# Performance work log

Hardware: AMD Instinct MI355X
Metric: run time of the kernel (lower is better)

Reference implementation:

```python
import jax, jax.numpy as jnp
import numpy as np

ATOMF_LEN = 82
EDGE_DIM = 6
HIDDEN = 10
GNN_DEPTH = 2
N_NODES = 200000
N_EDGES = 6400000


def _lrelu(x):
    return jax.nn.leaky_relu(x, negative_slope=0.1)


def setup_inputs() -> dict:
    key = jax.random.key(0)
    ks = jax.random.split(key, 7)
    vertex = jax.random.normal(ks[0], (N_NODES, ATOMF_LEN), dtype=jnp.float32)
    edge_feat = jax.random.normal(ks[1], (N_EDGES, EDGE_DIM), dtype=jnp.float32)
    src = jax.random.randint(ks[2], (N_EDGES,), 0, N_NODES, dtype=jnp.int32)
    dst = jax.random.randint(ks[3], (N_EDGES,), 0, N_NODES, dtype=jnp.int32)
    # kaiming-uniform-ish init scale (fan_in based)
    weight_init = jax.random.uniform(ks[4], (ATOMF_LEN, HIDDEN), dtype=jnp.float32,
                                     minval=-1.0, maxval=1.0) * (np.sqrt(6.0 / ATOMF_LEN))
    gather_weight = jax.random.uniform(ks[5], (HIDDEN + EDGE_DIM, HIDDEN), dtype=jnp.float32,
                                       minval=-1.0, maxval=1.0) * (np.sqrt(6.0 / (HIDDEN + EDGE_DIM)))
    update_weight = jax.random.uniform(ks[6], (2 * HIDDEN, HIDDEN), dtype=jnp.float32,
                                       minval=-1.0, maxval=1.0) * (np.sqrt(6.0 / (2 * HIDDEN)))
    return {"vertex": vertex, "edge_feat": edge_feat, "src": src, "dst": dst,
            "weight_init": weight_init, "gather_weight": gather_weight,
            "update_weight": update_weight}


def reference(vertex, edge_feat, src, dst, weight_init, gather_weight, update_weight):
    # embedding_: leaky_relu(mm(x, W), 0.1)
    h = _lrelu(vertex @ weight_init)  # [N, HIDDEN]
    n_nodes = vertex.shape[0]
    for _ in range(GNN_DEPTH):
        # gather: per-edge message from source node hidden + edge features
        msg = _lrelu(jnp.concatenate([h[src], edge_feat], axis=1) @ gather_weight)  # [E, HIDDEN]
        # scatter-sum aggregation onto destination nodes
        agg = jax.ops.segment_sum(msg, dst, num_segments=n_nodes)  # [N, HIDDEN]
        # update: combine current hidden with aggregated messages
        h = _lrelu(jnp.concatenate([h, agg], axis=1) @ update_weight)  # [N, HIDDEN]
    return h
```

## Files before the change

kernel.cpp:

```cpp
#include <hip/hip_runtime.h>

#define ATOMF 82
#define EDGE_DIM 6
#define HIDDEN 10
#define ZPAD 16

#define BSHIFT 8
#define BUCKN (1 << BSHIFT)
#define MAXBUCK 1024
#define NB2 256
#define MAXE3 16384

__device__ __forceinline__ float lrelu(float x) { return x > 0.f ? x : 0.1f * x; }

__device__ __forceinline__ unsigned int f2bf(float f) {
    unsigned int u = __float_as_uint(f);
    return (u + 0x7fffu + ((u >> 16) & 1u)) >> 16;
}
__device__ __forceinline__ float bf2f(unsigned int b) {
    return __uint_as_float(b << 16);
}

__global__ void embed_kernel(const float* __restrict__ vertex,
                             const float* __restrict__ W,
                             const float* __restrict__ GW,
                             float* __restrict__ h, unsigned short* __restrict__ z,
                             int n_nodes) {
    __shared__ float w[ATOMF * HIDDEN];
    __shared__ float gwh[HIDDEN * HIDDEN];
    for (int i = threadIdx.x; i < ATOMF * HIDDEN; i += blockDim.x) w[i] = W[i];
    for (int i = threadIdx.x; i < HIDDEN * HIDDEN; i += blockDim.x) gwh[i] = GW[i];
    __syncthreads();
    int node = blockIdx.x * blockDim.x + threadIdx.x;
    if (node >= n_nodes) return;
    const float2* v = (const float2*)(vertex + (long)node * ATOMF);
    float acc[HIDDEN];
#pragma unroll
    for (int j = 0; j < HIDDEN; j++) acc[j] = 0.f;
#pragma unroll 2
    for (int k2 = 0; k2 < ATOMF / 2; k2++) {
        float2 t = v[k2];
#pragma unroll
        for (int j = 0; j < HIDDEN; j++) acc[j] += t.x * w[(2 * k2) * HIDDEN + j];
#pragma unroll
        for (int j = 0; j < HIDDEN; j++) acc[j] += t.y * w[(2 * k2 + 1) * HIDDEN + j];
    }
    float ho[HIDDEN];
    float* out = h + (long)node * HIDDEN;
#pragma unroll
    for (int j = 0; j < HIDDEN; j++) { ho[j] = lrelu(acc[j]); out[j] = ho[j]; }
    float zv[HIDDEN];
#pragma unroll
    for (int j = 0; j < HIDDEN; j++) zv[j] = 0.f;
#pragma unroll
    for (int k = 0; k < HIDDEN; k++) {
        float x = ho[k];
#pragma unroll
        for (int j = 0; j < HIDDEN; j++) zv[j] += x * gwh[k * HIDDEN + j];
    }
    unsigned int* zq = (unsigned int*)(z + (size_t)node * ZPAD);
    int4 pk;
    pk.x = (int)(f2bf(zv[0]) | (f2bf(zv[1]) << 16));
    pk.y = (int)(f2bf(zv[2]) | (f2bf(zv[3]) << 16));
    pk.z = (int)(f2bf(zv[4]) | (f2bf(zv[5]) << 16));
    pk.w = (int)(f2bf(zv[6]) | (f2bf(zv[7]) << 16));
    *(int4*)zq = pk;
    zq[4] = f2bf(zv[8]) | (f2bf(zv[9]) << 16);
}

__global__ __launch_bounds__(512) void hist_kernel(const int* __restrict__ dst,
                                                   int* __restrict__ hist,
                                                   long n_edges, int nbuck) {
    __shared__ int hl[MAXBUCK];
    for (int t = threadIdx.x; t < nbuck; t += 512) hl[t] = 0;
    __syncthreads();
    long per = (n_edges + gridDim.x - 1) / gridDim.x;
    long s = (long)blockIdx.x * per;
    long e = s + per; if (e > n_edges) e = n_edges;
    for (long i = s + threadIdx.x; i < e; i += 512)
        atomicAdd(&hl[dst[i] >> BSHIFT], 1);
    __syncthreads();
    for (int t = threadIdx.x; t < nbuck; t += 512)
        hist[(size_t)t * gridDim.x + blockIdx.x] = hl[t];
}

__global__ __launch_bounds__(1024) void scan_block_sums(const int* __restrict__ in,
                                                        int* __restrict__ partials, int n) {
    __shared__ int ws[16];
    int i = blockIdx.x * 1024 + threadIdx.x;
    int v = (i < n) ? in[i] : 0;
    int lane = threadIdx.x & 63, wid = threadIdx.x >> 6;
    int s = v;
#pragma unroll
    for (int off = 32; off > 0; off >>= 1) s += __shfl_down(s, off, 64);
    if (lane == 0) ws[wid] = s;
    __syncthreads();
    if (threadIdx.x == 0) {
        int t = 0;
#pragma unroll
        for (int k = 0; k < 16; k++) t += ws[k];
        partials[blockIdx.x] = t;
    }
}
__global__ __launch_bounds__(1024) void scan_partials(int* __restrict__ partials, int nb) {
    __shared__ int wsum[16];
    int lane = threadIdx.x & 63, wid = threadIdx.x >> 6;
    int v = (threadIdx.x < nb) ? partials[threadIdx.x] : 0;
    int incl = v;
#pragma unroll
    for (int off = 1; off < 64; off <<= 1) {
        int t = __shfl_up(incl, off, 64);
        if (lane >= off) incl += t;
    }
    if (lane == 63) wsum[wid] = incl;
    __syncthreads();
    if (wid == 0 && lane < 16) {
        int wv = wsum[lane];
        int wincl = wv;
#pragma unroll
        for (int off = 1; off < 16; off <<= 1) {
            int t = __shfl_up(wincl, off, 64);
            if (lane >= off) wincl += t;
        }
        wsum[lane] = wincl - wv;
    }
    __syncthreads();
    if (threadIdx.x < nb) partials[threadIdx.x] = wsum[wid] + (incl - v);
}
__global__ __launch_bounds__(1024) void scan_final(const int* __restrict__ in,
                                                   const int* __restrict__ partials,
                                                   int* __restrict__ out, int n) {
    __shared__ int wsum[16];
    int i = blockIdx.x * 1024 + threadIdx.x;
    int v = (i < n) ? in[i] : 0;
    int lane = threadIdx.x & 63, wid = threadIdx.x >> 6;
    int incl = v;
#pragma unroll
    for (int off = 1; off < 64; off <<= 1) {
        int t = __shfl_up(incl, off, 64);
        if (lane >= off) incl += t;
    }
    if (lane == 63) wsum[wid] = incl;
    __syncthreads();
    if (wid == 0 && lane < 16) {
        int wv = wsum[lane];
        int wincl = wv;
#pragma unroll
        for (int off = 1; off < 16; off <<= 1) {
            int t = __shfl_up(wincl, off, 64);
            if (lane >= off) wincl += t;
        }
        wsum[lane] = wincl - wv;
    }
    __syncthreads();
    if (i <= n) out[i] = partials[blockIdx.x] + wsum[wid] + (incl - v);
}

__global__ __launch_bounds__(512) void part_scatter_kernel(
    const int* __restrict__ src, const int* __restrict__ dst,
    const float* __restrict__ ef, const int* __restrict__ base,
    int4* __restrict__ rec, long n_edges, int nbuck) {
    __shared__ int cur[MAXBUCK];
    for (int t = threadIdx.x; t < nbuck; t += 512)
        cur[t] = base[(size_t)t * gridDim.x + blockIdx.x];
    __syncthreads();
    long per = (n_edges + gridDim.x - 1) / gridDim.x;
    long s = (long)blockIdx.x * per;
    long e = s + per; if (e > n_edges) e = n_edges;
    for (long i = s + threadIdx.x; i < e; i += 512) {
        int d = dst[i];
        int slot = atomicAdd(&cur[d >> BSHIFT], 1);
        const float2* er = (const float2*)(ef + i * (long)EDGE_DIM);
        float2 fa = er[0], fb = er[1], fc = er[2];
        int4 r;
        r.x = src[i] | ((d & (BUCKN - 1)) << 24);
        r.y = (int)(f2bf(fa.x) | (f2bf(fa.y) << 16));
        r.z = (int)(f2bf(fb.x) | (f2bf(fb.y) << 16));
        r.w = (int)(f2bf(fc.x) | (f2bf(fc.y) << 16));
        rec[slot] = r;
    }
}

__global__ __launch_bounds__(256) void bucket_csr_kernel(
    const int* __restrict__ base, const int4* __restrict__ rec_a, int4* __restrict__ rec_b,
    int* __restrict__ offsets, int n_nodes) {
    __shared__ unsigned char lid[MAXE3];
    __shared__ int cnt[BUCKN];
    __shared__ int excl_s[BUCKN];
    __shared__ int cursor[BUCKN];
    int b = blockIdx.x;
    int S = base[(size_t)b * NB2];
    int E = base[(size_t)(b + 1) * NB2];
    int node0 = b << BSHIFT;
    int nn = n_nodes - node0; if (nn > BUCKN) nn = BUCKN;
    cnt[threadIdx.x] = 0;
    __syncthreads();
    int ne = E - S;
    bool fit = (ne <= MAXE3);
    for (int i = threadIdx.x; i < ne; i += 256) {
        int l = (int)((unsigned int)rec_a[S + i].x >> 24);
        if (fit) lid[i] = (unsigned char)l;
        atomicAdd(&cnt[l], 1);
    }
    __syncthreads();
    if (threadIdx.x == 0) {
        int run = 0;
#pragma unroll 4
        for (int l = 0; l < BUCKN; l++) { excl_s[l] = run; run += cnt[l]; }
    }
    __syncthreads();
    if ((int)threadIdx.x < nn) offsets[node0 + threadIdx.x] = S + excl_s[threadIdx.x];
    cursor[threadIdx.x] = excl_s[threadIdx.x];
    if (b == (int)gridDim.x - 1 && threadIdx.x == 0) offsets[n_nodes] = E;
    __syncthreads();
    for (int i = threadIdx.x; i < ne; i += 256) {
        int4 r = rec_a[S + i];
        int l = fit ? (int)lid[i] : (int)((unsigned int)r.x >> 24);
        int q = atomicAdd(&cursor[l], 1);
        rec_b[S + q] = r;
    }
}

__global__ void count_pos_kernel(const int* __restrict__ dst, int* __restrict__ counts,
                                 unsigned short* __restrict__ pos, long n_edges) {
    long e0 = ((long)blockIdx.x * blockDim.x + threadIdx.x) * 4;
    if (e0 + 3 < n_edges) {
        int4 d = *(const int4*)(dst + e0);
        ushort4 p;
        p.x = (unsigned short)atomicAdd(&counts[d.x], 1);
        p.y = (unsigned short)atomicAdd(&counts[d.y], 1);
        p.z = (unsigned short)atomicAdd(&counts[d.z], 1);
        p.w = (unsigned short)atomicAdd(&counts[d.w], 1);
        *(ushort4*)(pos + e0) = p;
    } else {
        for (long e = e0; e < n_edges; e++)
            pos[e] = (unsigned short)atomicAdd(&counts[dst[e]], 1);
    }
}
__global__ void scatter_rec_kernel(const int* __restrict__ src, const int* __restrict__ dst,
                                   const float* __restrict__ ef,
                                   const unsigned short* __restrict__ pos,
                                   const int* __restrict__ offsets,
                                   int4* __restrict__ rec, long n_edges) {
    long e = (long)blockIdx.x * blockDim.x + threadIdx.x;
    if (e >= n_edges) return;
    int d = dst[e];
    int q = offsets[d] + (int)pos[e];
    const float2* er = (const float2*)(ef + e * (long)EDGE_DIM);
    float2 fa = er[0], fb = er[1], fc = er[2];
    int4 r;
    r.x = src[e];
    r.y = (int)(f2bf(fa.x) | (f2bf(fa.y) << 16));
    r.z = (int)(f2bf(fb.x) | (f2bf(fb.y) << 16));
    r.w = (int)(f2bf(fc.x) | (f2bf(fc.y) << 16));
    rec[q] = r;
}

__global__ __launch_bounds__(256) void gather_update_kernel(
    const float* __restrict__ h_in, const unsigned short* __restrict__ z_in,
    const int4* __restrict__ rec, const int* __restrict__ offsets,
    const float* __restrict__ GW, const float* __restrict__ UW,
    float* __restrict__ h_out, unsigned short* __restrict__ z_out,
    int n_nodes, int write_z, unsigned int src_mask) {
    __shared__ float gwh[HIDDEN * HIDDEN];
    __shared__ float gwe[EDGE_DIM * HIDDEN];
    __shared__ float uw[2 * HIDDEN * HIDDEN];
    for (int i = threadIdx.x; i < HIDDEN * HIDDEN; i += 256) gwh[i] = GW[i];
    for (int i = threadIdx.x; i < EDGE_DIM * HIDDEN; i += 256) gwe[i] = GW[HIDDEN * HIDDEN + i];
    for (int i = threadIdx.x; i < 2 * HIDDEN * HIDDEN; i += 256) uw[i] = UW[i];
    __syncthreads();
    int group = threadIdx.x >> 4;
    int sub = threadIdx.x & 15;
    int node = blockIdx.x * 16 + group;
    if (node >= n_nodes) return;
    int off0 = offsets[node], off1 = offsets[node + 1];
    float acc[HIDDEN];
#pragma unroll
    for (int j = 0; j < HIDDEN; j++) acc[j] = 0.f;
    int p = off0 + sub;
    int4 r;
    if (p < off1) r = rec[p];
    while (p < off1) {
        int pn = p + 16;
        int4 rn = r;
        if (pn < off1) rn = rec[pn];
        int sn = (int)((unsigned int)r.x & src_mask);
        const int* zq = (const int*)(z_in + (size_t)sn * ZPAD);
        int4 za = *(const int4*)zq;
        int zb = zq[4];
        float ef[EDGE_DIM];
        unsigned int u0 = (unsigned int)r.y, u1 = (unsigned int)r.z, u2 = (unsigned int)r.w;
        ef[0] = bf2f(u0 & 0xffffu); ef[1] = bf2f(u0 >> 16);
        ef[2] = bf2f(u1 & 0xffffu); ef[3] = bf2f(u1 >> 16);
        ef[4] = bf2f(u2 & 0xffffu); ef[5] = bf2f(u2 >> 16);
        float m[HIDDEN];
#pragma unroll
        for (int j = 0; j < HIDDEN; j++) m[j] = 0.f;
#pragma unroll
        for (int k = 0; k < EDGE_DIM; k++) {
            float x = ef[k];
#pragma unroll
            for (int j = 0; j < HIDDEN; j++) m[j] += x * gwe[k * HIDDEN + j];
        }
        unsigned int z0 = (unsigned int)za.x, z1 = (unsigned int)za.y;
        unsigned int z2 = (unsigned int)za.z, z3 = (unsigned int)za.w, z4 = (unsigned int)zb;
        acc[0] += lrelu(m[0] + bf2f(z0 & 0xffffu));
        acc[1] += lrelu(m[1] + bf2f(z0 >> 16));
        acc[2] += lrelu(m[2] + bf2f(z1 & 0xffffu));
        acc[3] += lrelu(m[3] + bf2f(z1 >> 16));
        acc[4] += lrelu(m[4] + bf2f(z2 & 0xffffu));
        acc[5] += lrelu(m[5] + bf2f(z2 >> 16));
        acc[6] += lrelu(m[6] + bf2f(z3 & 0xffffu));
        acc[7] += lrelu(m[7] + bf2f(z3 >> 16));
        acc[8] += lrelu(m[8] + bf2f(z4 & 0xffffu));
        acc[9] += lrelu(m[9] + bf2f(z4 >> 16));
        r = rn; p = pn;
    }
#pragma unroll
    for (int j = 0; j < HIDDEN; j++) {
#pragma unroll
        for (int d = 8; d > 0; d >>= 1) acc[j] += __shfl_down(acc[j], d, 16);
    }
    if (sub == 0) {
        float in[2 * HIDDEN];
        const float2* hp = (const float2*)(h_in + (long)node * HIDDEN);
#pragma unroll
        for (int k = 0; k < 5; k++) { float2 t = hp[k]; in[2 * k] = t.x; in[2 * k + 1] = t.y; }
#pragma unroll
        for (int j = 0; j < HIDDEN; j++) in[HIDDEN + j] = acc[j];
        float o[HIDDEN];
#pragma unroll
        for (int j = 0; j < HIDDEN; j++) o[j] = 0.f;
#pragma unroll
        for (int k = 0; k < 2 * HIDDEN; k++) {
            float x = in[k];
#pragma unroll
            for (int j = 0; j < HIDDEN; j++) o[j] += x * uw[k * HIDDEN + j];
        }
        float ho[HIDDEN];
        float* outp = h_out + (long)node * HIDDEN;
#pragma unroll
        for (int j = 0; j < HIDDEN; j++) { ho[j] = lrelu(o[j]); outp[j] = ho[j]; }
        if (write_z) {
            float zv[HIDDEN];
#pragma unroll
            for (int j = 0; j < HIDDEN; j++) zv[j] = 0.f;
#pragma unroll
            for (int k = 0; k < HIDDEN; k++) {
                float x = ho[k];
#pragma unroll
                for (int j = 0; j < HIDDEN; j++) zv[j] += x * gwh[k * HIDDEN + j];
            }
            unsigned int* zq = (unsigned int*)(z_out + (size_t)node * ZPAD);
            int4 pk;
            pk.x = (int)(f2bf(zv[0]) | (f2bf(zv[1]) << 16));
            pk.y = (int)(f2bf(zv[2]) | (f2bf(zv[3]) << 16));
            pk.z = (int)(f2bf(zv[4]) | (f2bf(zv[5]) << 16));
            pk.w = (int)(f2bf(zv[6]) | (f2bf(zv[7]) << 16));
            *(int4*)zq = pk;
            zq[4] = f2bf(zv[8]) | (f2bf(zv[9]) << 16);
        }
    }
}

extern "C" void kernel_launch(void* const* d_in, const int* in_sizes, int n_in,
                              void* d_out, int out_size, void* d_ws, size_t ws_size,
                              hipStream_t stream) {
    const float* vertex    = (const float*)d_in[0];
    const float* edge_feat = (const float*)d_in[1];
    const int*   src       = (const int*)d_in[2];
    const int*   dst       = (const int*)d_in[3];
    const float* w_init    = (const float*)d_in[4];
    const float* gw        = (const float*)d_in[5];
    const float* uw        = (const float*)d_in[6];

    const int  n_nodes = in_sizes[0] / ATOMF;
    const long n_edges = (long)in_sizes[2];
    float* out = (float*)d_out;

    const int TB = 256;
    const int node_blocks = (n_nodes + TB - 1) / TB;
    const int gu_blocks   = (n_nodes + 15) / 16;

    const int nbuck = (n_nodes + BUCKN - 1) >> BSHIFT;
    const long m = (long)nbuck * NB2;
    const int scanb_m = (int)((m + 1 + 1023) / 1024);

    size_t tbl_bytes = (size_t)n_nodes * (2 * HIDDEN * sizeof(float) + 2 * ZPAD * sizeof(unsigned short));
    size_t rec_bytes = (size_t)n_edges * sizeof(int4);

    auto al = [](size_t x) { return (x + 255) & ~(size_t)255; };
    size_t need_new = al(m * 4) + al((m + 1) * 4) + al(2048 * 4) +
                      al((size_t)(n_nodes + 1) * 4) + al(rec_bytes) +
                      al(rec_bytes > tbl_bytes ? rec_bytes : tbl_bytes);

    char* ws = (char*)d_ws;
    size_t o = 0;
    auto alloc = [&](size_t bytes) { char* p = ws + o; o = (o + bytes + 255) & ~(size_t)255; return p; };

    if (nbuck <= MAXBUCK && scanb_m <= 1024 && n_nodes <= (1 << 24) && ws_size >= need_new) {
        int*  hist     = (int*)alloc(m * 4);
        int*  base     = (int*)alloc((m + 1) * 4);
        int*  partials = (int*)alloc(2048 * 4);
        int*  offsets  = (int*)alloc((size_t)(n_nodes + 1) * 4);
        int4* rec_b    = (int4*)alloc(rec_bytes);
        char* ovl      = alloc(rec_bytes > tbl_bytes ? rec_bytes : tbl_bytes);
        int4* rec_a    = (int4*)ovl;
        float*          h0 = (float*)ovl;
        float*          h1 = h0 + (size_t)n_nodes * HIDDEN;
        unsigned short* z0 = (unsigned short*)(h1 + (size_t)n_nodes * HIDDEN);
        unsigned short* z1 = z0 + (size_t)n_nodes * ZPAD;

        hist_kernel<<<NB2, 512, 0, stream>>>(dst, hist, n_edges, nbuck);
        scan_block_sums<<<scanb_m, 1024, 0, stream>>>(hist, partials, (int)m);
        scan_partials<<<1, 1024, 0, stream>>>(partials, scanb_m);
        scan_final<<<scanb_m, 1024, 0, stream>>>(hist, partials, base, (int)m);
        part_scatter_kernel<<<NB2, 512, 0, stream>>>(src, dst, edge_feat, base, rec_a,
                                                     n_edges, nbuck);
        bucket_csr_kernel<<<nbuck, 256, 0, stream>>>(base, rec_a, rec_b, offsets, n_nodes);

        embed_kernel<<<node_blocks, TB, 0, stream>>>(vertex, w_init, gw, h0, z0, n_nodes);
        gather_update_kernel<<<gu_blocks, TB, 0, stream>>>(h0, z0, rec_b, offsets, gw, uw,
                                                           h1, z1, n_nodes, 1, 0x00ffffffu);
        gather_update_kernel<<<gu_blocks, TB, 0, stream>>>(h1, z1, rec_b, offsets, gw, uw,
                                                           out, z0, n_nodes, 0, 0x00ffffffu);
    } else {
        int*  counts   = (int*)alloc((size_t)(n_nodes + 1) * 4);
        int*  offsets  = (int*)alloc((size_t)(n_nodes + 1) * 4);
        int*  partials = (int*)alloc(2048 * 4);
        int4* rec      = (int4*)alloc(rec_bytes);
        size_t pos_bytes = (size_t)n_edges * sizeof(unsigned short);
        char* overlay = alloc(pos_bytes > tbl_bytes ? pos_bytes : tbl_bytes);
        unsigned short* pos = (unsigned short*)overlay;
        float*          h0  = (float*)overlay;
        float*          h1  = h0 + (size_t)n_nodes * HIDDEN;
        unsigned short* z0  = (unsigned short*)(h1 + (size_t)n_nodes * HIDDEN);
        unsigned short* z1  = z0 + (size_t)n_nodes * ZPAD;

        const int edge_blocks = (int)((n_edges + TB - 1) / TB);
        const int cp_blocks   = (int)((n_edges / 4 + TB - 1) / TB);
        const int scan_blocks = (n_nodes + 1 + 1023) / 1024;

        hipMemsetAsync(counts, 0, (size_t)(n_nodes + 1) * 4, stream);
        count_pos_kernel<<<cp_blocks, TB, 0, stream>>>(dst, counts, pos, n_edges);
        scan_block_sums<<<scan_blocks, 1024, 0, stream>>>(counts, partials, n_nodes);
        scan_partials<<<1, 1024, 0, stream>>>(partials, scan_blocks);
        scan_final<<<scan_blocks, 1024, 0, stream>>>(counts, partials, offsets, n_nodes);
        scatter_rec_kernel<<<edge_blocks, TB, 0, stream>>>(src, dst, edge_feat, pos, offsets,
                                                           rec, n_edges);
        embed_kernel<<<node_blocks, TB, 0, stream>>>(vertex, w_init, gw, h0, z0, n_nodes);
        gather_update_kernel<<<gu_blocks, TB, 0, stream>>>(h0, z0, rec, offsets, gw, uw,
                                                           h1, z1, n_nodes, 1, 0xffffffffu);
        gather_update_kernel<<<gu_blocks, TB, 0, stream>>>(h1, z1, rec, offsets, gw, uw,
                                                           out, z0, n_nodes, 0, 0xffffffffu);
    }
    (void)ws_size;
}
```

Baseline: 760.7 us.

## Assign one thread per node in gather-update and vectorize partition scatter loads

Result: slower. 853.0 us (+12.1%).

```diff
diff --git a/kernel.cpp b/kernel.cpp
--- a/kernel.cpp
+++ b/kernel.cpp
@@ -164,20 +164,44 @@
     for (int t = threadIdx.x; t < nbuck; t += 512)
         cur[t] = base[(size_t)t * gridDim.x + blockIdx.x];
     __syncthreads();
-    long per = (n_edges + gridDim.x - 1) / gridDim.x;
+    long per = ((n_edges + gridDim.x - 1) / gridDim.x + 3) & ~3L;
     long s = (long)blockIdx.x * per;
     long e = s + per; if (e > n_edges) e = n_edges;
-    for (long i = s + threadIdx.x; i < e; i += 512) {
-        int d = dst[i];
-        int slot = atomicAdd(&cur[d >> BSHIFT], 1);
-        const float2* er = (const float2*)(ef + i * (long)EDGE_DIM);
-        float2 fa = er[0], fb = er[1], fc = er[2];
-        int4 r;
-        r.x = src[i] | ((d & (BUCKN - 1)) << 24);
-        r.y = (int)(f2bf(fa.x) | (f2bf(fa.y) << 16));
-        r.z = (int)(f2bf(fb.x) | (f2bf(fb.y) << 16));
-        r.w = (int)(f2bf(fc.x) | (f2bf(fc.y) << 16));
-        rec[slot] = r;
+    for (long i0 = s + (long)threadIdx.x * 4; i0 < e; i0 += 512 * 4) {
+        if (i0 + 3 < e) {
+            int4 d4 = *(const int4*)(dst + i0);
+            int4 s4 = *(const int4*)(src + i0);
+            int dd[4] = {d4.x, d4.y, d4.z, d4.w};
+            int ss[4] = {s4.x, s4.y, s4.z, s4.w};
+            int slot[4];
+#pragma unroll
+            for (int k = 0; k < 4; k++)
+                slot[k] = atomicAdd(&cur[dd[k] >> BSHIFT], 1);
+#pragma unroll
+            for (int k = 0; k < 4; k++) {
+                const float2* er = (const float2*)(ef + (i0 + k) * (long)EDGE_DIM);
+                float2 fa = er[0], fb = er[1], fc = er[2];
+                int4 r;
+                r.x = ss[k] | ((dd[k] & (BUCKN - 1)) << 24);
+                r.y = (int)(f2bf(fa.x) | (f2bf(fa.y) << 16));
+                r.z = (int)(f2bf(fb.x) | (f2bf(fb.y) << 16));
+                r.w = (int)(f2bf(fc.x) | (f2bf(fc.y) << 16));
+                rec[slot[k]] = r;
+            }
+        } else {
+            for (long i = i0; i < e; i++) {
+                int d = dst[i];
+                int slot = atomicAdd(&cur[d >> BSHIFT], 1);
+                const float2* er = (const float2*)(ef + i * (long)EDGE_DIM);
+                float2 fa = er[0], fb = er[1], fc = er[2];
+                int4 r;
+                r.x = src[i] | ((d & (BUCKN - 1)) << 24);
+                r.y = (int)(f2bf(fa.x) | (f2bf(fa.y) << 16));
+                r.z = (int)(f2bf(fb.x) | (f2bf(fb.y) << 16));
+                r.w = (int)(f2bf(fc.x) | (f2bf(fc.y) << 16));
+                rec[slot] = r;
+            }
+        }
     }
 }
 
@@ -269,97 +293,94 @@
     for (int i = threadIdx.x; i < EDGE_DIM * HIDDEN; i += 256) gwe[i] = GW[HIDDEN * HIDDEN + i];
     for (int i = threadIdx.x; i < 2 * HIDDEN * HIDDEN; i += 256) uw[i] = UW[i];
     __syncthreads();
-    int group = threadIdx.x >> 4;
-    int sub = threadIdx.x & 15;
-    int node = blockIdx.x * 16 + group;
+    int node = blockIdx.x * 256 + threadIdx.x;
     if (node >= n_nodes) return;
     int off0 = offsets[node], off1 = offsets[node + 1];
     float acc[HIDDEN];
 #pragma unroll
     for (int j = 0; j < HIDDEN; j++) acc[j] = 0.f;
-    int p = off0 + sub;
-    int4 r;
-    if (p < off1) r = rec[p];
-    while (p < off1) {
-        int pn = p + 16;
-        int4 rn = r;
-        if (pn < off1) rn = rec[pn];
-        int sn = (int)((unsigned int)r.x & src_mask);
-        const int* zq = (const int*)(z_in + (size_t)sn * ZPAD);
-        int4 za = *(const int4*)zq;
-        int zb = zq[4];
-        float ef[EDGE_DIM];
-        unsigned int u0 = (unsigned int)r.y, u1 = (unsigned int)r.z, u2 = (unsigned int)r.w;
-        ef[0] = bf2f(u0 & 0xffffu); ef[1] = bf2f(u0 >> 16);
-        ef[2] = bf2f(u1 & 0xffffu); ef[3] = bf2f(u1 >> 16);
-        ef[4] = bf2f(u2 & 0xffffu); ef[5] = bf2f(u2 >> 16);
-        float m[HIDDEN];
-#pragma unroll
-        for (int j = 0; j < HIDDEN; j++) m[j] = 0.f;
-#pragma unroll
-        for (int k = 0; k < EDGE_DIM; k++) {
-            float x = ef[k];
-#pragma unroll
-            for (int j = 0; j < HIDDEN; j++) m[j] += x * gwe[k * HIDDEN + j];
-        }
-        unsigned int z0 = (unsigned int)za.x, z1 = (unsigned int)za.y;
-        unsigned int z2 = (unsigned int)za.z, z3 = (unsigned int)za.w, z4 = (unsigned int)zb;
-        acc[0] += lrelu(m[0] + bf2f(z0 & 0xffffu));
-        acc[1] += lrelu(m[1] + bf2f(z0 >> 16));
-        acc[2] += lrelu(m[2] + bf2f(z1 & 0xffffu));
-        acc[3] += lrelu(m[3] + bf2f(z1 >> 16));
-        acc[4] += lrelu(m[4] + bf2f(z2 & 0xffffu));
-        acc[5] += lrelu(m[5] + bf2f(z2 >> 16));
-        acc[6] += lrelu(m[6] + bf2f(z3 & 0xffffu));
-        acc[7] += lrelu(m[7] + bf2f(z3 >> 16));
-        acc[8] += lrelu(m[8] + bf2f(z4 & 0xffffu));
-        acc[9] += lrelu(m[9] + bf2f(z4 >> 16));
-        r = rn; p = pn;
-    }
-#pragma unroll
-    for (int j = 0; j < HIDDEN; j++) {
-#pragma unroll
-        for (int d = 8; d > 0; d >>= 1) acc[j] += __shfl_down(acc[j], d, 16);
-    }
-    if (sub == 0) {
-        float in[2 * HIDDEN];
-        const float2* hp = (const float2*)(h_in + (long)node * HIDDEN);
-#pragma unroll
-        for (int k = 0; k < 5; k++) { float2 t = hp[k]; in[2 * k] = t.x; in[2 * k + 1] = t.y; }
-#pragma unroll
-        for (int j = 0; j < HIDDEN; j++) in[HIDDEN + j] = acc[j];
-        float o[HIDDEN];
-#pragma unroll
-        for (int j = 0; j < HIDDEN; j++) o[j] = 0.f;
-#pragma unroll
-        for (int k = 0; k < 2 * HIDDEN; k++) {
-            float x = in[k];
-#pragma unroll
-            for (int j = 0; j < HIDDEN; j++) o[j] += x * uw[k * HIDDEN + j];
-        }
-        float ho[HIDDEN];
-        float* outp = h_out + (long)node * HIDDEN;
-#pragma unroll
-        for (int j = 0; j < HIDDEN; j++) { ho[j] = lrelu(o[j]); outp[j] = ho[j]; }
-        if (write_z) {
-            float zv[HIDDEN];
-#pragma unroll
-            for (int j = 0; j < HIDDEN; j++) zv[j] = 0.f;
-#pragma unroll
-            for (int k = 0; k < HIDDEN; k++) {
-                float x = ho[k];
-#pragma unroll
-                for (int j = 0; j < HIDDEN; j++) zv[j] += x * gwh[k * HIDDEN + j];
+    for (int p = off0; p < off1; p += 4) {
+        int nb = off1 - p;
+        int4 r[4];
+#pragma unroll
+        for (int k = 0; k < 4; k++) if (k < nb) r[k] = rec[p + k];
+        int4 za[4]; int zb[4];
+#pragma unroll
+        for (int k = 0; k < 4; k++) if (k < nb) {
+            const int* zq = (const int*)(z_in +
+                (size_t)((unsigned int)r[k].x & src_mask) * ZPAD);
+            za[k] = *(const int4*)zq;
+            zb[k] = zq[4];
+        }
+#pragma unroll
+        for (int k = 0; k < 4; k++) if (k < nb) {
+            float ef[EDGE_DIM];
+            unsigned int u0 = (unsigned int)r[k].y, u1 = (unsigned int)r[k].z,
+                         u2 = (unsigned int)r[k].w;
+            ef[0] = bf2f(u0 & 0xffffu); ef[1] = bf2f(u0 >> 16);
+            ef[2] = bf2f(u1 & 0xffffu); ef[3] = bf2f(u1 >> 16);
+            ef[4] = bf2f(u2 & 0xffffu); ef[5] = bf2f(u2 >> 16);
+            float m[HIDDEN];
+#pragma unroll
+            for (int j = 0; j < HIDDEN; j++) m[j] = 0.f;
+#pragma unroll
+            for (int kk = 0; kk < EDGE_DIM; kk++) {
+                float x = ef[kk];
+#pragma unroll
+                for (int j = 0; j < HIDDEN; j++) m[j] += x * gwe[kk * HIDDEN + j];
             }
-            unsigned int* zq = (unsigned int*)(z_out + (size_t)node * ZPAD);
-            int4 pk;
-            pk.x = (int)(f2bf(zv[0]) | (f2bf(zv[1]) << 16));
-            pk.y = (int)(f2bf(zv[2]) | (f2bf(zv[3]) << 16));
-            pk.z = (int)(f2bf(zv[4]) | (f2bf(zv[5]) << 16));
-            pk.w = (int)(f2bf(zv[6]) | (f2bf(zv[7]) << 16));
-            *(int4*)zq = pk;
-            zq[4] = f2bf(zv[8]) | (f2bf(zv[9]) << 16);
-        }
+            unsigned int z0 = (unsigned int)za[k].x, z1 = (unsigned int)za[k].y;
+            unsigned int z2 = (unsigned int)za[k].z, z3 = (unsigned int)za[k].w;
+            unsigned int z4 = (unsigned int)zb[k];
+            acc[0] += lrelu(m[0] + bf2f(z0 & 0xffffu));
+            acc[1] += lrelu(m[1] + bf2f(z0 >> 16));
+            acc[2] += lrelu(m[2] + bf2f(z1 & 0xffffu));
+            acc[3] += lrelu(m[3] + bf2f(z1 >> 16));
+            acc[4] += lrelu(m[4] + bf2f(z2 & 0xffffu));
+            acc[5] += lrelu(m[5] + bf2f(z2 >> 16));
+            acc[6] += lrelu(m[6] + bf2f(z3 & 0xffffu));
+            acc[7] += lrelu(m[7] + bf2f(z3 >> 16));
+            acc[8] += lrelu(m[8] + bf2f(z4 & 0xffffu));
+            acc[9] += lrelu(m[9] + bf2f(z4 >> 16));
+        }
+    }
+    float in[2 * HIDDEN];
+    const float2* hp = (const float2*)(h_in + (size_t)node * HIDDEN);
+#pragma unroll
+    for (int k = 0; k < 5; k++) { float2 t = hp[k]; in[2 * k] = t.x; in[2 * k + 1] = t.y; }
+#pragma unroll
+    for (int j = 0; j < HIDDEN; j++) in[HIDDEN + j] = acc[j];
+    float o[HIDDEN];
+#pragma unroll
+    for (int j = 0; j < HIDDEN; j++) o[j] = 0.f;
+#pragma unroll
+    for (int k = 0; k < 2 * HIDDEN; k++) {
+        float x = in[k];
+#pragma unroll
+        for (int j = 0; j < HIDDEN; j++) o[j] += x * uw[k * HIDDEN + j];
+    }
+    float ho[HIDDEN];
+    float* outp = h_out + (size_t)node * HIDDEN;
+#pragma unroll
+    for (int j = 0; j < HIDDEN; j++) { ho[j] = lrelu(o[j]); outp[j] = ho[j]; }
+    if (write_z) {
+        float zv[HIDDEN];
+#pragma unroll
+        for (int j = 0; j < HIDDEN; j++) zv[j] = 0.f;
+#pragma unroll
+        for (int k = 0; k < HIDDEN; k++) {
+            float x = ho[k];
+#pragma unroll
+            for (int j = 0; j < HIDDEN; j++) zv[j] += x * gwh[k * HIDDEN + j];
+        }
+        unsigned int* zq = (unsigned int*)(z_out + (size_t)node * ZPAD);
+        int4 pk;
+        pk.x = (int)(f2bf(zv[0]) | (f2bf(zv[1]) << 16));
+        pk.y = (int)(f2bf(zv[2]) | (f2bf(zv[3]) << 16));
+        pk.z = (int)(f2bf(zv[4]) | (f2bf(zv[5]) << 16));
+        pk.w = (int)(f2bf(zv[6]) | (f2bf(zv[7]) << 16));
+        *(int4*)zq = pk;
+        zq[4] = f2bf(zv[8]) | (f2bf(zv[9]) << 16);
     }
 }
 
@@ -380,7 +401,7 @@
 
     const int TB = 256;
     const int node_blocks = (n_nodes + TB - 1) / TB;
-    const int gu_blocks   = (n_nodes + 15) / 16;
+    const int gu_blocks   = (n_nodes + 255) / 256;
 
     const int nbuck = (n_nodes + BUCKN - 1) >> BSHIFT;
     const long m = (long)nbuck * NB2;
@@ -420,10 +441,10 @@
         bucket_csr_kernel<<<nbuck, 256, 0, stream>>>(base, rec_a, rec_b, offsets, n_nodes);
 
         embed_kernel<<<node_blocks, TB, 0, stream>>>(vertex, w_init, gw, h0, z0, n_nodes);
-        gather_update_kernel<<<gu_blocks, TB, 0, stream>>>(h0, z0, rec_b, offsets, gw, uw,
-                                                           h1, z1, n_nodes, 1, 0x00ffffffu);
-        gather_update_kernel<<<gu_blocks, TB, 0, stream>>>(h1, z1, rec_b, offsets, gw, uw,
-                                                           out, z0, n_nodes, 0, 0x00ffffffu);
+        gather_update_kernel<<<gu_blocks, 256, 0, stream>>>(h0, z0, rec_b, offsets, gw, uw,
+                                                            h1, z1, n_nodes, 1, 0x00ffffffu);
+        gather_update_kernel<<<gu_blocks, 256, 0, stream>>>(h1, z1, rec_b, offsets, gw, uw,
+                                                            out, z0, n_nodes, 0, 0x00ffffffu);
     } else {
         int*  counts   = (int*)alloc((size_t)(n_nodes + 1) * 4);
         int*  offsets  = (int*)alloc((size_t)(n_nodes + 1) * 4);
@@ -449,10 +470,10 @@
         scatter_rec_kernel<<<edge_blocks, TB, 0, stream>>>(src, dst, edge_feat, pos, offsets,
                                                            rec, n_edges);
         embed_kernel<<<node_blocks, TB, 0, stream>>>(vertex, w_init, gw, h0, z0, n_nodes);
-        gather_update_kernel<<<gu_blocks, TB, 0, stream>>>(h0, z0, rec, offsets, gw, uw,
-                                                           h1, z1, n_nodes, 1, 0xffffffffu);
-        gather_update_kernel<<<gu_blocks, TB, 0, stream>>>(h1, z1, rec, offsets, gw, uw,
-                                                           out, z0, n_nodes, 0, 0xffffffffu);
+        gather_update_kernel<<<gu_blocks, 256, 0, stream>>>(h0, z0, rec, offsets, gw, uw,
+                                                            h1, z1, n_nodes, 1, 0xffffffffu);
+        gather_update_kernel<<<gu_blocks, 256, 0, stream>>>(h1, z1, rec, offsets, gw, uw,
+                                                            out, z0, n_nodes, 0, 0xffffffffu);
     }
     (void)ws_size;
 }
```
